# Optimization experiments

Measured on AMD Instinct MI355X. Metric: run time of the kernel, lower is better.

Reference implementation:

```python
import jax, jax.numpy as jnp
import numpy as np

B, S, D = 2, 2048, 1024
H = 16
HD = D // H  # 64

def setup_inputs() -> dict:
    key = jax.random.key(0)
    ks = jax.random.split(key, 6)
    scale = 0.02
    x   = jax.random.normal(ks[0], (B, S, D), dtype=jnp.float32)
    Wq  = jax.random.normal(ks[1], (D, D), dtype=jnp.float32) * scale
    Wk  = jax.random.normal(ks[2], (D, D), dtype=jnp.float32) * scale
    Wv  = jax.random.normal(ks[3], (D, D), dtype=jnp.float32) * scale
    Wo  = jax.random.normal(ks[4], (D, D), dtype=jnp.float32) * scale
    bo  = jax.random.normal(ks[5], (D,), dtype=jnp.float32) * scale
    return {"x": x, "Wq": Wq, "Wk": Wk, "Wv": Wv, "Wo": Wo, "bo": bo}

def reference(x, Wq, Wk, Wv, Wo, bo):
    b, s, d = x.shape
    # QKV projections (no bias, qkv_bias=False); weights stored as [d_in, d_out]
    q = (x @ Wq).reshape(b, s, H, HD).transpose(0, 2, 1, 3)  # [b,h,s,hd]
    k = (x @ Wk).reshape(b, s, H, HD).transpose(0, 2, 1, 3)
    v = (x @ Wv).reshape(b, s, H, HD).transpose(0, 2, 1, 3)
    scores = jnp.einsum('bhqd,bhkd->bhqk', q, k)  # [b,h,s,s]
    causal = jnp.triu(jnp.ones((s, s), dtype=bool), k=1)
    scores = jnp.where(causal, -jnp.inf, scores)
    attn = jax.nn.softmax(scores / jnp.sqrt(jnp.float32(HD)), axis=-1)
    # dropout_rate = 0.0 -> identity
    ctx = jnp.einsum('bhqk,bhkd->bqhd', attn, v).reshape(b, s, d)
    return ctx @ Wo + bo
```

## Files before the change

kernel.cpp:

```cpp
#include <hip/hip_runtime.h>
#include <hip/hip_bf16.h>
#include <math.h>

#define B_ 2
#define S_ 2048
#define D_ 1024
#define H_ 16
#define HD_ 64
#define M_ (B_*S_)

typedef __attribute__((ext_vector_type(8))) short bf16x8;
typedef __attribute__((ext_vector_type(4))) float f32x4;

#define MFMA16(a,b,c) __builtin_amdgcn_mfma_f32_16x16x32_bf16(a,b,c,0,0,0)
#define INFF __builtin_inff()
#define LOG2E 1.44269504088896340736f
#define EXP2F(x) __builtin_amdgcn_exp2f(x)

static __device__ __forceinline__ unsigned short f2bf_bits(float f) {
    unsigned int u = __float_as_uint(f);
    unsigned int r = (u + 0x7fffu + ((u >> 16) & 1u)) >> 16;
    return (unsigned short)r;
}

static __device__ __forceinline__ unsigned cvt_pk_bf16(float a, float b) {
    unsigned r;
    asm("v_cvt_pk_bf16_f32 %0, %1, %2" : "=v"(r) : "v"(a), "v"(b));
    return r;
}

static __device__ __forceinline__ void gload16(const unsigned short* g, unsigned short* l) {
    __builtin_amdgcn_global_load_lds(
        (const __attribute__((address_space(1))) unsigned int*)(g),
        (__attribute__((address_space(3))) unsigned int*)(l),
        16, 0, 0);
}

#define BARR do { \
    __builtin_amdgcn_sched_barrier(0); \
    __builtin_amdgcn_s_barrier(); \
    __builtin_amdgcn_sched_barrier(0); \
} while (0)
#define LGK0 do { \
    asm volatile("s_waitcnt lgkmcnt(0)" ::: "memory"); \
    __builtin_amdgcn_sched_barrier(0); \
} while (0)
#define LGK8 do { \
    asm volatile("s_waitcnt lgkmcnt(8)" ::: "memory"); \
    __builtin_amdgcn_sched_barrier(0); \
} while (0)
#define VM0 do { \
    asm volatile("s_waitcnt vmcnt(0)" ::: "memory"); \
    __builtin_amdgcn_sched_barrier(0); \
} while (0)
#define VM4 do { \
    asm volatile("s_waitcnt vmcnt(4)" ::: "memory"); \
    __builtin_amdgcn_sched_barrier(0); \
} while (0)
#define VM6 do { \
    asm volatile("s_waitcnt vmcnt(6)" ::: "memory"); \
    __builtin_amdgcn_sched_barrier(0); \
} while (0)

__global__ __launch_bounds__(256) void convert_x_kernel(
    const float* __restrict__ x, unsigned short* __restrict__ o) {
    size_t i = (size_t)blockIdx.x * 256 + threadIdx.x;
    float4 v = reinterpret_cast<const float4*>(x)[i];
    ushort4 u;
    u.x = f2bf_bits(v.x); u.y = f2bf_bits(v.y);
    u.z = f2bf_bits(v.z); u.w = f2bf_bits(v.w);
    reinterpret_cast<ushort4*>(o)[i] = u;
}

__global__ __launch_bounds__(256) void convw_kernel(
    const float* __restrict__ W0, const float* __restrict__ W1,
    const float* __restrict__ W2, const float* __restrict__ W3,
    unsigned short* __restrict__ OT) {
    __shared__ float t[32][33];
    const float* W = (blockIdx.z == 0) ? W0 : (blockIdx.z == 1) ? W1
                    : (blockIdx.z == 2) ? W2 : W3;
    unsigned short* O = OT + (size_t)blockIdx.z * D_ * D_;
    int tx = threadIdx.x & 31, ty = threadIdx.x >> 5;
    int kb = blockIdx.y * 32, nb = blockIdx.x * 32;
#pragma unroll
    for (int i = 0; i < 4; i++)
        t[ty + 8*i][tx] = W[(size_t)(kb + ty + 8*i) * D_ + nb + tx];
    __syncthreads();
#pragma unroll
    for (int i = 0; i < 4; i++) {
        int n = nb + ty + 8*i, k = kb + tx;
        O[(size_t)n * D_ + k] = f2bf_bits(t[tx][ty + 8*i]);
    }
}

__global__ __launch_bounds__(512, 2) void gemm_qkv256(
    const unsigned short* __restrict__ A,
    const unsigned short* __restrict__ BT,
    unsigned short* __restrict__ outp)
{
    __shared__ union {
        struct { unsigned short A[2][2][8192]; unsigned short B[2][2][8192]; } s;
        unsigned short vt[256][136];
    } sm;
    const int tid = threadIdx.x, lane = tid & 63, wid = tid >> 6;
    const int lrow = lane & 15, lk8 = lane >> 4, orow = lk8 * 4;
    const int wmo = (wid >> 2) * 64;
    const int wno = (wid & 3) * 32;
    const int m0 = blockIdx.x * 256, n0 = blockIdx.y * 256;

    const int srow = lane >> 3, sgr = lane & 7;
    const unsigned sgo = (unsigned)(wid * 8 + srow) * 1024u
                       + (unsigned)((sgr ^ srow) << 3);
    const unsigned short* Ag = A  + (unsigned)m0 * 1024u + sgo;
    const unsigned short* Bg = BT + (unsigned)n0 * 1024u + sgo;
    const int ldsrb = wid * 512;

    const int sw0 = ((lk8 ^ (lrow & 7)) << 3);
    const int sw1 = (((4 | lk8) ^ (lrow & 7)) << 3);
    int ar[4], br[2];
#pragma unroll
    for (int f = 0; f < 4; f++) ar[f] = (wmo + f * 16 + lrow) * 64;
#pragma unroll
    for (int g = 0; g < 2; g++) br[g] = (wno + g * 16 + lrow) * 64;

    f32x4 acc[8][4] = {};
    bf16x8 af[4][2], bf0[2][2], bf1[2][2];

    auto stA = [&](int par, int mh, unsigned k) {
        unsigned short* d = &sm.s.A[par][mh][ldsrb];
        const unsigned short* g = Ag + (unsigned)mh * 131072u + k;
        gload16(g, d);
        gload16(g + 65536u, d + 4096);
    };
    auto stB = [&](int par, int nh, unsigned k) {
        unsigned short* d = &sm.s.B[par][nh][ldsrb];
        const unsigned short* g = Bg + (unsigned)nh * 131072u + k;
        gload16(g, d);
        gload16(g + 65536u, d + 4096);
    };
    auto lda = [&](int par, int mh) {
        const unsigned short* p = &sm.s.A[par][mh][0];
#pragma unroll
        for (int f = 0; f < 4; f++) {
            af[f][0] = *reinterpret_cast<const bf16x8*>(p + ar[f] + sw0);
            af[f][1] = *reinterpret_cast<const bf16x8*>(p + ar[f] + sw1);
        }
    };
    auto ldb0 = [&](int par, int nh) {
        const unsigned short* p = &sm.s.B[par][nh][0];
#pragma unroll
        for (int g = 0; g < 2; g++) {
            bf0[g][0] = *reinterpret_cast<const bf16x8*>(p + br[g] + sw0);
            bf0[g][1] = *reinterpret_cast<const bf16x8*>(p + br[g] + sw1);
        }
    };
    auto ldb1 = [&](int par, int nh) {
        const unsigned short* p = &sm.s.B[par][nh][0];
#pragma unroll
        for (int g = 0; g < 2; g++) {
            bf1[g][0] = *reinterpret_cast<const bf16x8*>(p + br[g] + sw0);
            bf1[g][1] = *reinterpret_cast<const bf16x8*>(p + br[g] + sw1);
        }
    };
    auto MMA0 = [&](int mh) {
        __builtin_amdgcn_s_setprio(1);
#pragma unroll
        for (int f = 0; f < 4; f++)
#pragma unroll
            for (int g = 0; g < 2; g++)
#pragma unroll
                for (int ks = 0; ks < 2; ks++)
                    acc[mh*4+f][g] = MFMA16(af[f][ks], bf0[g][ks], acc[mh*4+f][g]);
        __builtin_amdgcn_s_setprio(0);
    };
    auto MMA1 = [&](int mh) {
        __builtin_amdgcn_s_setprio(1);
#pragma unroll
        for (int f = 0; f < 4; f++)
#pragma unroll
            for (int g = 0; g < 2; g++)
#pragma unroll
                for (int ks = 0; ks < 2; ks++)
                    acc[mh*4+f][2+g] = MFMA16(af[f][ks], bf1[g][ks], acc[mh*4+f][2+g]);
        __builtin_amdgcn_s_setprio(0);
    };

    stA(0, 0, 0);  stB(0, 0, 0);  stB(0, 1, 0);  stA(0, 1, 0);
    stA(1, 0, 64); stB(1, 0, 64); stB(1, 1, 64);
    VM6; BARR;

#pragma unroll 1
    for (int i = 0; i < 8; i++) {
        const unsigned kA1 = (unsigned)(2*i + 1) * 64u;
        const unsigned k2  = (unsigned)((2*i + 2) & 15) * 64u;
        const unsigned k3  = (unsigned)((2*i + 3) & 15) * 64u;
        lda(0, 0); ldb0(0, 0); stA(1, 1, kA1);
        LGK8; BARR; LGK0; MMA0(0); BARR;
        ldb1(0, 1); stA(0, 0, k2);
        BARR; LGK0; MMA1(0); BARR;
        lda(0, 1); stB(0, 0, k2);
        BARR; LGK0; MMA1(1); BARR;
        stB(0, 1, k2);
        VM6; BARR; MMA0(1); BARR;
        lda(1, 0); ldb0(1, 0); stA(0, 1, k2);
        LGK8; BARR; LGK0; MMA0(0); BARR;
        ldb1(1, 1); stA(1, 0, k3);
        BARR; LGK0; MMA1(0); BARR;
        lda(1, 1); stB(1, 0, k3);
        BARR; LGK0; MMA1(1); BARR;
        stB(1, 1, k3);
        VM6; BARR; MMA0(1); BARR;
    }

    asm volatile("s_waitcnt vmcnt(0)" ::: "memory");
    __builtin_amdgcn_sched_barrier(0);
    __builtin_amdgcn_s_barrier();

    const int which = n0 >> 10;
    const int nl0 = n0 & 1023;
    const int bq = m0 >> 11;
    unsigned short* obase = outp + (size_t)which * 4194304;

    if (which < 2) {
        const float scale = (which == 0) ? (0.125f * LOG2E) : 1.0f;
#pragma unroll
        for (int fi = 0; fi < 8; fi++)
#pragma unroll
            for (int g = 0; g < 4; g++)
#pragma unroll
                for (int r = 0; r < 4; r++) {
                    int m = m0 + (fi >> 2) * 128 + wmo + (fi & 3) * 16 + orow + r;
                    int n = nl0 + (g >> 1) * 128 + wno + (g & 1) * 16 + lrow;
                    int s = m & 2047;
                    obase[(((size_t)(bq * 16 + (n >> 6)) * 2048 + s) << 6) + (n & 63)]
                        = f2bf_bits(acc[fi][g][r] * scale);
                }
    } else {
#pragma unroll
        for (int qm = 0; qm < 2; qm++) {
#pragma unroll
            for (int f = 0; f < 4; f++)
#pragma unroll
                for (int g = 0; g < 4; g++) {
                    const int ml = wmo + f * 16 + orow;
                    const int nc = (g >> 1) * 128 + wno + (g & 1) * 16 + lrow;
                    uint2 w;
                    w.x = cvt_pk_bf16(acc[qm*4+f][g][0], acc[qm*4+f][g][1]);
                    w.y = cvt_pk_bf16(acc[qm*4+f][g][2], acc[qm*4+f][g][3]);
                    *reinterpret_cast<uint2*>(&sm.vt[nc][ml]) = w;
                }
            __syncthreads();
            {
                const int row = tid >> 1, c0 = (tid & 1) * 64;
                unsigned short* dst = obase +
                    ((size_t)(bq * 1024) + nl0 + row) * 2048 +
                    (m0 & 2047) + qm * 128 + c0;
#pragma unroll
                for (int j = 0; j < 64; j += 8)
                    *reinterpret_cast<bf16x8*>(dst + j) =
                        *reinterpret_cast<const bf16x8*>(&sm.vt[row][c0 + j]);
            }
            __syncthreads();
        }
    }
}

template<int BN, int MODE>
__global__ __launch_bounds__(256) void gemm_gl(
    const unsigned short* __restrict__ A,
    const unsigned short* __restrict__ BT,
    void* __restrict__ outp,
    const float* __restrict__ bias)
{
    constexpr int K = 1024;
    constexpr int NF = (BN == 128) ? 4 : 2;
    __shared__ struct { unsigned short As[128][64]; unsigned short Bs[BN][64]; } sm;
    const int m0 = blockIdx.x * 128;
    const int n0 = blockIdx.y * BN;
    const int tid = threadIdx.x, lane = tid & 63, wid = tid >> 6;
    const int wm = (wid >> 1) * 64;
    const int wn = (wid & 1) * (BN / 2);
    const int lrow = lane & 15, lk8 = lane >> 4, orow = lk8 * 4;
    f32x4 acc[4][NF] = {};

    for (int k0 = 0; k0 < K; k0 += 64) {
#pragma unroll
        for (int i = 0; i < 4; i++) {
            const int rbase = wid * 32 + i * 8;
            const int rl = rbase + (lane >> 3);
            const int sc = ((lane & 7) ^ (rl & 7)) << 3;
            gload16(A + (size_t)(m0 + rl) * K + k0 + sc, &sm.As[rbase][0]);
        }
#pragma unroll
        for (int i = 0; i < BN / 32; i++) {
            const int rbase = wid * (BN / 4) + i * 8;
            const int rl = rbase + (lane >> 3);
            const int sc = ((lane & 7) ^ (rl & 7)) << 3;
            gload16(BT + (size_t)(n0 + rl) * K + k0 + sc, &sm.Bs[rbase][0]);
        }
        __syncthreads();
#pragma unroll
        for (int ks = 0; ks < 2; ks++) {
            bf16x8 af[4], bfr[NF];
#pragma unroll
            for (int f = 0; f < 4; f++) {
                const int row = wm + f * 16 + lrow;
                const int p = (ks * 4 + lk8) ^ (row & 7);
                af[f] = *reinterpret_cast<const bf16x8*>(&sm.As[row][p * 8]);
            }
#pragma unroll
            for (int f = 0; f < NF; f++) {
                const int row = wn + f * 16 + lrow;
                const int p = (ks * 4 + lk8) ^ (row & 7);
                bfr[f] = *reinterpret_cast<const bf16x8*>(&sm.Bs[row][p * 8]);
            }
            __builtin_amdgcn_s_setprio(1);
#pragma unroll
            for (int mf = 0; mf < 4; mf++)
#pragma unroll
                for (int nf = 0; nf < NF; nf++)
                    acc[mf][nf] = MFMA16(af[mf], bfr[nf], acc[mf][nf]);
            __builtin_amdgcn_s_setprio(0);
        }
        __syncthreads();
    }

    float* o = (float*)outp;
#pragma unroll
    for (int mf = 0; mf < 4; mf++)
#pragma unroll
        for (int nf = 0; nf < NF; nf++)
#pragma unroll
            for (int r = 0; r < 4; r++) {
                int m = m0 + wm + mf*16 + orow + r;
                int n = n0 + wn + nf*16 + lrow;
                o[(size_t)m * 1024 + n] = acc[mf][nf][r] + bias[n];
            }
}

__global__ __launch_bounds__(256, 3) void attn_kernel(
    const unsigned short* __restrict__ Q,
    const unsigned short* __restrict__ Kb,
    const unsigned short* __restrict__ VT,
    unsigned short* __restrict__ ctx)
{
    __shared__ unsigned short Ks[3][64][64];
    __shared__ unsigned short Vs[3][64][64];
    const int fid = blockIdx.x;
    const int xcd = fid & 7, t = fid >> 3;
    const int bh = xcd | ((t & 3) << 3);
    const int qt = 31 - (t >> 2);
    const int lane = threadIdx.x & 63, wid = threadIdx.x >> 6;
    const int lrow = lane & 15, lk8 = lane >> 4, orow = lk8 * 4;
    const unsigned short* Qp = Q  + (size_t)bh * (S_ * 64);
    const unsigned short* Kp = Kb + (size_t)bh * (S_ * 64);
    const unsigned short* Vp = VT + (size_t)bh * (64 * S_);
    const int b = bh >> 4, h = bh & 15;
    const int q0 = qt * 64 + wid * 16;
    const int nb = qt + 1;

    auto stage = [&](int buf, int kv0) {
#pragma unroll
        for (int i = 0; i < 2; i++) {
            const int rbase = wid * 16 + 8 * i;
            const int rl = rbase + (lane >> 3);
            const int sc = (((lane & 7) ^ (rl & 7)) << 3);
            gload16(Kp + (size_t)(kv0 + rl) * 64 + sc, &Ks[buf][rbase][0]);
            gload16(Vp + (size_t)rl * S_ + kv0 + sc, &Vs[buf][rbase][0]);
        }
    };

    stage(0, 0);
    stage(1, 64);

    bf16x8 qf[2];
#pragma unroll
    for (int kt = 0; kt < 2; kt++)
        qf[kt] = *reinterpret_cast<const bf16x8*>(
            Qp + (size_t)(q0 + lrow) * 64 + kt*32 + lk8*8);

    f32x4 acc[4] = {};
    float lr = 0.f;

    VM4;
    BARR;

    int cur = 0, n2 = 2;
#pragma unroll 1
    for (int kvb = 0; kvb < nb; kvb++) {
        if (kvb + 2 < nb) stage(n2, (kvb + 2) * 64);

        f32x4 sacc[4] = {};
        __builtin_amdgcn_s_setprio(1);
#pragma unroll
        for (int kt = 0; kt < 2; kt++)
#pragma unroll
            for (int nf = 0; nf < 4; nf++) {
                const int row = nf * 16 + lrow;
                const int g = ((kt << 2) | lk8) ^ (row & 7);
                bf16x8 kf = *reinterpret_cast<const bf16x8*>(&Ks[cur][row][g << 3]);
                sacc[nf] = MFMA16(kf, qf[kt], sacc[nf]);
            }
        __builtin_amdgcn_s_setprio(0);
        if (kvb == qt) {
#pragma unroll
            for (int nf = 0; nf < 4; nf++)
#pragma unroll
                for (int r = 0; r < 4; r++)
                    if (nf*16 + orow + r > wid*16 + lrow) sacc[nf][r] = -INFF;
        }
        float ps[4];
#pragma unroll
        for (int nf = 0; nf < 4; nf++) {
#pragma unroll
            for (int r = 0; r < 4; r++)
                sacc[nf][r] = EXP2F(sacc[nf][r]);
            ps[nf] = (sacc[nf][0] + sacc[nf][1]) + (sacc[nf][2] + sacc[nf][3]);
        }
        lr += (ps[0] + ps[1]) + (ps[2] + ps[3]);

        bf16x8 pf[2];
#pragma unroll
        for (int kt = 0; kt < 2; kt++) {
            unsigned a0 = cvt_pk_bf16(sacc[2*kt][0],   sacc[2*kt][1]);
            unsigned a1 = cvt_pk_bf16(sacc[2*kt][2],   sacc[2*kt][3]);
            unsigned b0 = cvt_pk_bf16(sacc[2*kt+1][0], sacc[2*kt+1][1]);
            unsigned b1 = cvt_pk_bf16(sacc[2*kt+1][2], sacc[2*kt+1][3]);
            asm("v_permlane32_swap_b32 %0, %1" : "+v"(a0), "+v"(b0));
            asm("v_permlane16_swap_b32 %0, %1" : "+v"(a0), "+v"(b0));
            asm("v_permlane32_swap_b32 %0, %1" : "+v"(a1), "+v"(b1));
            asm("v_permlane16_swap_b32 %0, %1" : "+v"(a1), "+v"(b1));
            union { unsigned u[4]; bf16x8 v; } pk;
            pk.u[0] = a0; pk.u[1] = a1; pk.u[2] = b0; pk.u[3] = b1;
            pf[kt] = pk.v;
        }

        __builtin_amdgcn_s_setprio(1);
#pragma unroll
        for (int kt = 0; kt < 2; kt++)
#pragma unroll
            for (int nf = 0; nf < 4; nf++) {
                const int row = nf * 16 + lrow;
                const int g = ((kt << 2) | lk8) ^ (row & 7);
                bf16x8 vf = *reinterpret_cast<const bf16x8*>(&Vs[cur][row][g << 3]);
                acc[nf] = MFMA16(pf[kt], vf, acc[nf]);
            }
        __builtin_amdgcn_s_setprio(0);

        if (kvb + 1 < nb) {
            if (kvb + 2 < nb) { VM4; } else { VM0; }
            BARR;
        }
        cur = (cur == 2) ? 0 : cur + 1;
        n2  = (n2  == 2) ? 0 : n2  + 1;
    }

    asm volatile("s_waitcnt vmcnt(0)" ::: "memory");

    lr += __shfl_xor(lr, 16);
    lr += __shfl_xor(lr, 32);
    const float inv = 1.0f / lr;
#pragma unroll
    for (int r = 0; r < 4; r++) {
        const float linv = __shfl(inv, (lane & 48) + orow + r);
#pragma unroll
        for (int nf = 0; nf < 4; nf++) {
            int s = q0 + orow + r;
            int col = h * 64 + nf * 16 + lrow;
            ctx[((size_t)(b * S_ + s)) * D_ + col] = f2bf_bits(acc[nf][r] * linv);
        }
    }
}

extern "C" void kernel_launch(void* const* d_in, const int* in_sizes, int n_in,
                              void* d_out, int out_size, void* d_ws, size_t ws_size,
                              hipStream_t stream) {
    const float* x  = (const float*)d_in[0];
    const float* Wq = (const float*)d_in[1];
    const float* Wk = (const float*)d_in[2];
    const float* Wv = (const float*)d_in[3];
    const float* Wo = (const float*)d_in[4];
    const float* bo = (const float*)d_in[5];
    float* out = (float*)d_out;

    char* ws = (char*)d_ws;
    unsigned short* xb  = (unsigned short*)(ws);
    unsigned short* WT  = (unsigned short*)(ws + 8388608);
    unsigned short* QKV = (unsigned short*)(ws + 16777216);
    unsigned short* ctx = (unsigned short*)(ws + 41943040);

    unsigned short* Qb  = QKV;
    unsigned short* Kb  = QKV + 4194304;
    unsigned short* VTb = QKV + 8388608;

    convert_x_kernel<<<dim3(4096), dim3(256), 0, stream>>>(x, xb);
    convw_kernel<<<dim3(32, 32, 4), dim3(256), 0, stream>>>(Wq, Wk, Wv, Wo, WT);

    gemm_qkv256<<<dim3(16, 12), dim3(512), 0, stream>>>(xb, WT, QKV);

    attn_kernel<<<dim3(1024), dim3(256), 0, stream>>>(Qb, Kb, VTb, ctx);

    gemm_gl<64, 1><<<dim3(32, 16), dim3(256), 0, stream>>>(
        ctx, WT + 3145728, (void*)out, bo);
}
```

Before: 100.9 us.

## Pair short and long causal query tiles per attention block for load balance

Each attention block now handles two query tiles, p and 31-p, so every block does the same amount of causal work. Both tiles share one staged K/V stream, so each K/V tile loaded into shared memory feeds two sets of MFMAs while the short tile is still active. The grid is halved to 512 blocks, with launch bounds lowered to 2 blocks per CU to leave room for the doubled accumulators and Q fragments. The costs are higher register pressure, lower occupancy and extra branching on whether the short tile is still active.

Measured after the change: 105.2 us. +4.3%, slower.

```diff
diff --git a/kernel.cpp b/kernel.cpp
--- a/kernel.cpp
+++ b/kernel.cpp
@@ -338,7 +338,7 @@
             }
 }
 
-__global__ __launch_bounds__(256, 3) void attn_kernel(
+__global__ __launch_bounds__(256, 2) void attn_kernel(
     const unsigned short* __restrict__ Q,
     const unsigned short* __restrict__ Kb,
     const unsigned short* __restrict__ VT,
@@ -349,15 +349,17 @@
     const int fid = blockIdx.x;
     const int xcd = fid & 7, t = fid >> 3;
     const int bh = xcd | ((t & 3) << 3);
-    const int qt = 31 - (t >> 2);
+    const int p  = t >> 2;
+    const int qtA = p, qtB = 31 - p;
     const int lane = threadIdx.x & 63, wid = threadIdx.x >> 6;
     const int lrow = lane & 15, lk8 = lane >> 4, orow = lk8 * 4;
     const unsigned short* Qp = Q  + (size_t)bh * (S_ * 64);
     const unsigned short* Kp = Kb + (size_t)bh * (S_ * 64);
     const unsigned short* Vp = VT + (size_t)bh * (64 * S_);
     const int b = bh >> 4, h = bh & 15;
-    const int q0 = qt * 64 + wid * 16;
-    const int nb = qt + 1;
+    const int q0A = qtA * 64 + wid * 16;
+    const int q0B = qtB * 64 + wid * 16;
+    const int nb = qtB + 1;
 
     auto stage = [&](int buf, int kv0) {
 #pragma unroll
@@ -373,14 +375,17 @@
     stage(0, 0);
     stage(1, 64);
 
-    bf16x8 qf[2];
-#pragma unroll
-    for (int kt = 0; kt < 2; kt++)
-        qf[kt] = *reinterpret_cast<const bf16x8*>(
-            Qp + (size_t)(q0 + lrow) * 64 + kt*32 + lk8*8);
-
-    f32x4 acc[4] = {};
-    float lr = 0.f;
+    bf16x8 qfA[2], qfB[2];
+#pragma unroll
+    for (int kt = 0; kt < 2; kt++) {
+        qfA[kt] = *reinterpret_cast<const bf16x8*>(
+            Qp + (size_t)(q0A + lrow) * 64 + kt*32 + lk8*8);
+        qfB[kt] = *reinterpret_cast<const bf16x8*>(
+            Qp + (size_t)(q0B + lrow) * 64 + kt*32 + lk8*8);
+    }
+
+    f32x4 accA[4] = {}, accB[4] = {};
+    float lrA = 0.f, lrB = 0.f;
 
     VM4;
     BARR;
@@ -389,62 +394,124 @@
 #pragma unroll 1
     for (int kvb = 0; kvb < nb; kvb++) {
         if (kvb + 2 < nb) stage(n2, (kvb + 2) * 64);
-
-        f32x4 sacc[4] = {};
+        const bool aAct = (kvb <= qtA);
+
+        f32x4 sA[4] = {}, sB[4] = {};
         __builtin_amdgcn_s_setprio(1);
-#pragma unroll
-        for (int kt = 0; kt < 2; kt++)
+        if (aAct) {
+#pragma unroll
+            for (int kt = 0; kt < 2; kt++)
+#pragma unroll
+                for (int nf = 0; nf < 4; nf++) {
+                    const int row = nf * 16 + lrow;
+                    const int g = ((kt << 2) | lk8) ^ (row & 7);
+                    bf16x8 kf = *reinterpret_cast<const bf16x8*>(&Ks[cur][row][g << 3]);
+                    sB[nf] = MFMA16(kf, qfB[kt], sB[nf]);
+                    sA[nf] = MFMA16(kf, qfA[kt], sA[nf]);
+                }
+        } else {
+#pragma unroll
+            for (int kt = 0; kt < 2; kt++)
+#pragma unroll
+                for (int nf = 0; nf < 4; nf++) {
+                    const int row = nf * 16 + lrow;
+                    const int g = ((kt << 2) | lk8) ^ (row & 7);
+                    bf16x8 kf = *reinterpret_cast<const bf16x8*>(&Ks[cur][row][g << 3]);
+                    sB[nf] = MFMA16(kf, qfB[kt], sB[nf]);
+                }
+        }
+        __builtin_amdgcn_s_setprio(0);
+
+        if (kvb == qtB) {
+#pragma unroll
+            for (int nf = 0; nf < 4; nf++)
+#pragma unroll
+                for (int r = 0; r < 4; r++)
+                    if (nf*16 + orow + r > wid*16 + lrow) sB[nf][r] = -INFF;
+        }
+        if (aAct && kvb == qtA) {
+#pragma unroll
+            for (int nf = 0; nf < 4; nf++)
+#pragma unroll
+                for (int r = 0; r < 4; r++)
+                    if (nf*16 + orow + r > wid*16 + lrow) sA[nf][r] = -INFF;
+        }
+
+        bf16x8 pfB[2], pfA[2];
+        {
+            float ps[4];
 #pragma unroll
             for (int nf = 0; nf < 4; nf++) {
-                const int row = nf * 16 + lrow;
-                const int g = ((kt << 2) | lk8) ^ (row & 7);
-                bf16x8 kf = *reinterpret_cast<const bf16x8*>(&Ks[cur][row][g << 3]);
-                sacc[nf] = MFMA16(kf, qf[kt], sacc[nf]);
-            }
-        __builtin_amdgcn_s_setprio(0);
-        if (kvb == qt) {
-#pragma unroll
-            for (int nf = 0; nf < 4; nf++)
 #pragma unroll
                 for (int r = 0; r < 4; r++)
-                    if (nf*16 + orow + r > wid*16 + lrow) sacc[nf][r] = -INFF;
-        }
-        float ps[4];
-#pragma unroll
-        for (int nf = 0; nf < 4; nf++) {
-#pragma unroll
-            for (int r = 0; r < 4; r++)
-                sacc[nf][r] = EXP2F(sacc[nf][r]);
-            ps[nf] = (sacc[nf][0] + sacc[nf][1]) + (sacc[nf][2] + sacc[nf][3]);
-        }
-        lr += (ps[0] + ps[1]) + (ps[2] + ps[3]);
-
-        bf16x8 pf[2];
-#pragma unroll
-        for (int kt = 0; kt < 2; kt++) {
-            unsigned a0 = cvt_pk_bf16(sacc[2*kt][0],   sacc[2*kt][1]);
-            unsigned a1 = cvt_pk_bf16(sacc[2*kt][2],   sacc[2*kt][3]);
-            unsigned b0 = cvt_pk_bf16(sacc[2*kt+1][0], sacc[2*kt+1][1]);
-            unsigned b1 = cvt_pk_bf16(sacc[2*kt+1][2], sacc[2*kt+1][3]);
-            asm("v_permlane32_swap_b32 %0, %1" : "+v"(a0), "+v"(b0));
-            asm("v_permlane16_swap_b32 %0, %1" : "+v"(a0), "+v"(b0));
-            asm("v_permlane32_swap_b32 %0, %1" : "+v"(a1), "+v"(b1));
-            asm("v_permlane16_swap_b32 %0, %1" : "+v"(a1), "+v"(b1));
-            union { unsigned u[4]; bf16x8 v; } pk;
-            pk.u[0] = a0; pk.u[1] = a1; pk.u[2] = b0; pk.u[3] = b1;
-            pf[kt] = pk.v;
+                    sB[nf][r] = EXP2F(sB[nf][r]);
+                ps[nf] = (sB[nf][0] + sB[nf][1]) + (sB[nf][2] + sB[nf][3]);
+            }
+            lrB += (ps[0] + ps[1]) + (ps[2] + ps[3]);
+#pragma unroll
+            for (int kt = 0; kt < 2; kt++) {
+                unsigned a0 = cvt_pk_bf16(sB[2*kt][0],   sB[2*kt][1]);
+                unsigned a1 = cvt_pk_bf16(sB[2*kt][2],   sB[2*kt][3]);
+                unsigned b0 = cvt_pk_bf16(sB[2*kt+1][0], sB[2*kt+1][1]);
+                unsigned b1 = cvt_pk_bf16(sB[2*kt+1][2], sB[2*kt+1][3]);
+                asm("v_permlane32_swap_b32 %0, %1" : "+v"(a0), "+v"(b0));
+                asm("v_permlane16_swap_b32 %0, %1" : "+v"(a0), "+v"(b0));
+                asm("v_permlane32_swap_b32 %0, %1" : "+v"(a1), "+v"(b1));
+                asm("v_permlane16_swap_b32 %0, %1" : "+v"(a1), "+v"(b1));
+                union { unsigned u[4]; bf16x8 v; } pk;
+                pk.u[0] = a0; pk.u[1] = a1; pk.u[2] = b0; pk.u[3] = b1;
+                pfB[kt] = pk.v;
+            }
+        }
+        if (aAct) {
+            float ps[4];
+#pragma unroll
+            for (int nf = 0; nf < 4; nf++) {
+#pragma unroll
+                for (int r = 0; r < 4; r++)
+                    sA[nf][r] = EXP2F(sA[nf][r]);
+                ps[nf] = (sA[nf][0] + sA[nf][1]) + (sA[nf][2] + sA[nf][3]);
+            }
+            lrA += (ps[0] + ps[1]) + (ps[2] + ps[3]);
+#pragma unroll
+            for (int kt = 0; kt < 2; kt++) {
+                unsigned a0 = cvt_pk_bf16(sA[2*kt][0],   sA[2*kt][1]);
+                unsigned a1 = cvt_pk_bf16(sA[2*kt][2],   sA[2*kt][3]);
+                unsigned b0 = cvt_pk_bf16(sA[2*kt+1][0], sA[2*kt+1][1]);
+                unsigned b1 = cvt_pk_bf16(sA[2*kt+1][2], sA[2*kt+1][3]);
+                asm("v_permlane32_swap_b32 %0, %1" : "+v"(a0), "+v"(b0));
+                asm("v_permlane16_swap_b32 %0, %1" : "+v"(a0), "+v"(b0));
+                asm("v_permlane32_swap_b32 %0, %1" : "+v"(a1), "+v"(b1));
+                asm("v_permlane16_swap_b32 %0, %1" : "+v"(a1), "+v"(b1));
+                union { unsigned u[4]; bf16x8 v; } pk;
+                pk.u[0] = a0; pk.u[1] = a1; pk.u[2] = b0; pk.u[3] = b1;
+                pfA[kt] = pk.v;
+            }
         }
 
         __builtin_amdgcn_s_setprio(1);
-#pragma unroll
-        for (int kt = 0; kt < 2; kt++)
-#pragma unroll
-            for (int nf = 0; nf < 4; nf++) {
-                const int row = nf * 16 + lrow;
-                const int g = ((kt << 2) | lk8) ^ (row & 7);
-                bf16x8 vf = *reinterpret_cast<const bf16x8*>(&Vs[cur][row][g << 3]);
-                acc[nf] = MFMA16(pf[kt], vf, acc[nf]);
-            }
+        if (aAct) {
+#pragma unroll
+            for (int kt = 0; kt < 2; kt++)
+#pragma unroll
+                for (int nf = 0; nf < 4; nf++) {
+                    const int row = nf * 16 + lrow;
+                    const int g = ((kt << 2) | lk8) ^ (row & 7);
+                    bf16x8 vf = *reinterpret_cast<const bf16x8*>(&Vs[cur][row][g << 3]);
+                    accB[nf] = MFMA16(pfB[kt], vf, accB[nf]);
+                    accA[nf] = MFMA16(pfA[kt], vf, accA[nf]);
+                }
+        } else {
+#pragma unroll
+            for (int kt = 0; kt < 2; kt++)
+#pragma unroll
+                for (int nf = 0; nf < 4; nf++) {
+                    const int row = nf * 16 + lrow;
+                    const int g = ((kt << 2) | lk8) ^ (row & 7);
+                    bf16x8 vf = *reinterpret_cast<const bf16x8*>(&Vs[cur][row][g << 3]);
+                    accB[nf] = MFMA16(pfB[kt], vf, accB[nf]);
+                }
+        }
         __builtin_amdgcn_s_setprio(0);
 
         if (kvb + 1 < nb) {
@@ -457,17 +524,23 @@
 
     asm volatile("s_waitcnt vmcnt(0)" ::: "memory");
 
-    lr += __shfl_xor(lr, 16);
-    lr += __shfl_xor(lr, 32);
-    const float inv = 1.0f / lr;
+    lrA += __shfl_xor(lrA, 16);
+    lrA += __shfl_xor(lrA, 32);
+    lrB += __shfl_xor(lrB, 16);
+    lrB += __shfl_xor(lrB, 32);
+    const float invA = 1.0f / lrA;
+    const float invB = 1.0f / lrB;
 #pragma unroll
     for (int r = 0; r < 4; r++) {
-        const float linv = __shfl(inv, (lane & 48) + orow + r);
+        const float liA = __shfl(invA, (lane & 48) + orow + r);
+        const float liB = __shfl(invB, (lane & 48) + orow + r);
 #pragma unroll
         for (int nf = 0; nf < 4; nf++) {
-            int s = q0 + orow + r;
-            int col = h * 64 + nf * 16 + lrow;
-            ctx[((size_t)(b * S_ + s)) * D_ + col] = f2bf_bits(acc[nf][r] * linv);
+            const int col = h * 64 + nf * 16 + lrow;
+            ctx[((size_t)(b * S_ + q0A + orow + r)) * D_ + col]
+                = f2bf_bits(accA[nf][r] * liA);
+            ctx[((size_t)(b * S_ + q0B + orow + r)) * D_ + col]
+                = f2bf_bits(accB[nf][r] * liB);
         }
     }
 }
@@ -498,7 +571,7 @@
 
     gemm_qkv256<<<dim3(16, 12), dim3(512), 0, stream>>>(xb, WT, QKV);
 
-    attn_kernel<<<dim3(1024), dim3(256), 0, stream>>>(Qb, Kb, VTb, ctx);
+    attn_kernel<<<dim3(512), dim3(256), 0, stream>>>(Qb, Kb, VTb, ctx);
 
     gemm_gl<64, 1><<<dim3(32, 16), dim3(256), 0, stream>>>(
         ctx, WT + 3145728, (void*)out, bo);
```
